# Kernel optimization log

Measured on AMD Instinct MI355X. Metric: run time of the kernel, lower is better.

## Reference

```python
import jax, jax.numpy as jnp
import numpy as np

N_NODES = 50000


def gcn_conv(x, row, col, ew, W, b, n_nodes):
    """PyG GCNConv: add self-loops, symmetric normalization, scatter-add aggregation."""
    loop = jnp.arange(n_nodes)
    r = jnp.concatenate([row, loop])
    c = jnp.concatenate([col, loop])
    w = jnp.concatenate([ew, jnp.ones((n_nodes,), ew.dtype)])
    deg = jax.ops.segment_sum(w, c, num_segments=n_nodes)          # [N]
    dinv = jnp.where(deg > 0, jax.lax.rsqrt(deg), 0.0)
    norm = dinv[r] * w * dinv[c]                                   # [E+N]
    h = x @ W                                                      # [N, out]
    msg = h[r] * norm[:, None]                                     # [E+N, out]
    out = jax.ops.segment_sum(msg, c, num_segments=n_nodes)        # [N, out]
    return out + b


def setup_inputs() -> dict:
    key = jax.random.key(0)
    ks = jax.random.split(key, 7)
    n_feats, hidden, n_classes, n_edges = 256, 128, 40, 800000
    x = jax.random.normal(ks[0], (N_NODES, n_feats), dtype=jnp.float32)
    edge_index = jax.random.randint(ks[1], (2, n_edges), 0, N_NODES, dtype=jnp.int64)
    edge_weight = jax.random.uniform(ks[2], (n_edges,), dtype=jnp.float32)
    # Glorot-ish init for the two GCNConv linear layers (weight stored as [in, out])
    W1 = jax.random.normal(ks[3], (n_feats, hidden), dtype=jnp.float32) * (1.0 / np.sqrt(n_feats))
    b1 = jnp.zeros((hidden,), dtype=jnp.float32)
    W2 = jax.random.normal(ks[4], (hidden, n_classes), dtype=jnp.float32) * (1.0 / np.sqrt(hidden))
    b2 = jnp.zeros((n_classes,), dtype=jnp.float32)
    return {"x": x, "edge_index": edge_index, "edge_weight": edge_weight,
            "W1": W1, "b1": b1, "W2": W2, "b2": b2}


def reference(x, edge_index, edge_weight, W1, b1, W2, b2):
    # Dropout is identity in eval mode.
    row, col = edge_index[0], edge_index[1]
    h = gcn_conv(x, row, col, edge_weight, W1, b1, N_NODES)
    h = jax.nn.relu(h)
    out = gcn_conv(h, row, col, edge_weight, W2, b2, N_NODES)
    return out
```

## Files before the change

kernel.cpp:

```cpp
#include <hip/hip_runtime.h>

#define N_FEATS 256
#define HIDDEN  128
#define NCLASS  40
#define H2PAD   48
#define ELLCAP  64

typedef __attribute__((ext_vector_type(8))) short short8;
typedef __attribute__((ext_vector_type(4))) float f32x4;

static __device__ __forceinline__ unsigned short f2bf(float f) {
    unsigned u = __float_as_uint(f);
    u += 0x7fffu + ((u >> 16) & 1u);
    return (unsigned short)(u >> 16);
}
static __device__ __forceinline__ float bflo(unsigned u) { return __uint_as_float(u << 16); }
static __device__ __forceinline__ float bfhi(unsigned u) { return __uint_as_float(u & 0xffff0000u); }

static __device__ __forceinline__ unsigned wq16(float w) {
    float q = w * 65536.0f + 0.5f;
    q = fminf(q, 65535.0f);
    return (unsigned)q;
}
#define WDEQ (1.0f / 65536.0f)

__global__ void k_convW(const float* __restrict__ W1, const float* __restrict__ W2,
                        unsigned short* __restrict__ Wp, unsigned short* __restrict__ Wp2,
                        unsigned long long* __restrict__ cntw, int N) {
    int idx = blockIdx.x * 256 + threadIdx.x;
    if (idx < N) cntw[idx] = 0ull;
    if (idx < N_FEATS * HIDDEN) {
        int n = idx >> 8, k = idx & 255;
        Wp[idx] = f2bf(W1[(size_t)k * HIDDEN + n]);
    } else {
        int j = idx - N_FEATS * HIDDEN;
        if (j < H2PAD * HIDDEN) {
            int n = j >> 7, k = j & 127;
            Wp2[j] = (n < NCLASS) ? f2bf(W2[(size_t)k * NCLASS + n]) : 0;
        }
    }
}

__global__ __launch_bounds__(256) void k_fat(const float* __restrict__ x,
                                             const unsigned short* __restrict__ Wp,
                                             unsigned short* __restrict__ C,
                                             const int* __restrict__ col,
                                             const int* __restrict__ row,
                                             const float* __restrict__ ew,
                                             unsigned long long* __restrict__ cntw,
                                             unsigned* __restrict__ ed,
                                             int GB, int CB, int N, int E) {
    int bid = blockIdx.x;
    int M = GB < CB ? GB : CB;
    int tile = -1, chunk = -1;
    if (bid < 2 * M) {
        if (bid & 1) chunk = bid >> 1; else tile = bid >> 1;
    } else {
        int r = bid - 2 * M;
        if (GB > CB) tile = M + r; else chunk = M + r;
    }

    if (tile >= 0) {
        __shared__ unsigned short Als[64][72];
        __shared__ unsigned short Bls[128][72];
        int t = threadIdx.x;
        int r0 = tile * 64;
        int wave = t >> 6, lane = t & 63;
        int ml = lane & 15, qd = lane >> 4;

        f32x4 acc[8];
        #pragma unroll
        for (int i = 0; i < 8; ++i) acc[i] = (f32x4){0.f, 0.f, 0.f, 0.f};

        int arow = t >> 2, akg = t & 3;
        int bn = t >> 1, bkg = t & 1;

        for (int k0 = 0; k0 < N_FEATS; k0 += 32) {
            {
                float4 xa0 = make_float4(0.f, 0.f, 0.f, 0.f), xa1 = xa0;
                if (r0 + arow < N) {
                    const float* src = &x[(size_t)(r0 + arow) * N_FEATS + k0 + akg * 8];
                    xa0 = *(const float4*)src;
                    xa1 = *(const float4*)(src + 4);
                }
                short8 av;
                av[0] = (short)f2bf(xa0.x); av[1] = (short)f2bf(xa0.y);
                av[2] = (short)f2bf(xa0.z); av[3] = (short)f2bf(xa0.w);
                av[4] = (short)f2bf(xa1.x); av[5] = (short)f2bf(xa1.y);
                av[6] = (short)f2bf(xa1.z); av[7] = (short)f2bf(xa1.w);
                *(short8*)&Als[arow][akg * 8] = av;
            }
            {
                const short8* src = (const short8*)&Wp[(size_t)bn * N_FEATS + k0 + bkg * 16];
                *(short8*)&Bls[bn][bkg * 16]     = src[0];
                *(short8*)&Bls[bn][bkg * 16 + 8] = src[1];
            }
            __syncthreads();
            short8 af = *(const short8*)&Als[wave * 16 + ml][qd * 8];
            #pragma unroll
            for (int nt = 0; nt < 8; ++nt) {
                short8 bf = *(const short8*)&Bls[nt * 16 + ml][qd * 8];
                acc[nt] = __builtin_amdgcn_mfma_f32_16x16x32_bf16(af, bf, acc[nt], 0, 0, 0);
            }
            __syncthreads();
        }
        #pragma unroll
        for (int nt = 0; nt < 8; ++nt) {
            int q = nt >> 1;
            int fo = (nt & 1) * 16 + ml;
            #pragma unroll
            for (int r = 0; r < 4; ++r) {
                int grow = r0 + wave * 16 + qd * 4 + r;
                if (grow < N)
                    C[(size_t)q * N * 32 + (size_t)grow * 32 + fo] = (unsigned short)f2bf(acc[nt][r]);
            }
        }
    } else {
        int base = chunk * 1024 + threadIdx.x * 4;
        if (base + 4 <= E) {
            int4   c4 = *(const int4*)&col[base];
            int4   r4 = *(const int4*)&row[base];
            float4 w4 = *(const float4*)&ew[base];
            unsigned q0 = wq16(w4.x), q1 = wq16(w4.y), q2 = wq16(w4.z), q3 = wq16(w4.w);
            unsigned p0 = ((unsigned)r4.x << 16) | q0;
            unsigned p1 = ((unsigned)r4.y << 16) | q1;
            unsigned p2 = ((unsigned)r4.z << 16) | q2;
            unsigned p3 = ((unsigned)r4.w << 16) | q3;
            unsigned long long a0 = atomicAdd(&cntw[c4.x], ((unsigned long long)q0 << 20) | 1ull);
            unsigned long long a1 = atomicAdd(&cntw[c4.y], ((unsigned long long)q1 << 20) | 1ull);
            unsigned long long a2 = atomicAdd(&cntw[c4.z], ((unsigned long long)q2 << 20) | 1ull);
            unsigned long long a3 = atomicAdd(&cntw[c4.w], ((unsigned long long)q3 << 20) | 1ull);
            int s0 = (int)(a0 & 0xFFFFFu);
            int s1 = (int)(a1 & 0xFFFFFu);
            int s2 = (int)(a2 & 0xFFFFFu);
            int s3 = (int)(a3 & 0xFFFFFu);
            if (s0 < ELLCAP) __builtin_nontemporal_store(p0, &ed[((size_t)c4.x << 6) + s0]);
            if (s1 < ELLCAP) __builtin_nontemporal_store(p1, &ed[((size_t)c4.y << 6) + s1]);
            if (s2 < ELLCAP) __builtin_nontemporal_store(p2, &ed[((size_t)c4.z << 6) + s2]);
            if (s3 < ELLCAP) __builtin_nontemporal_store(p3, &ed[((size_t)c4.w << 6) + s3]);
        } else {
            for (int e = base; e < E; ++e) {
                int c = col[e];
                unsigned q = wq16(ew[e]);
                unsigned p = ((unsigned)row[e] << 16) | q;
                unsigned long long a = atomicAdd(&cntw[c], ((unsigned long long)q << 20) | 1ull);
                int s = (int)(a & 0xFFFFFu);
                if (s < ELLCAP) __builtin_nontemporal_store(p, &ed[((size_t)c << 6) + s]);
            }
        }
    }
}

__global__ void k_degdinv(const unsigned long long* __restrict__ cntw,
                          float* __restrict__ dinv, int* __restrict__ cnt, int N) {
    int c = blockIdx.x * blockDim.x + threadIdx.x;
    if (c >= N) return;
    unsigned long long v = cntw[c];
    int m = (int)(v & 0xFFFFFu); if (m > ELLCAP) m = ELLCAP;
    cnt[c] = m;
    dinv[c] = rsqrtf(1.0f + (float)(v >> 20) * WDEQ);
}

__global__ __launch_bounds__(256) void k_gather1(const int* __restrict__ cnt,
                                                 const unsigned* __restrict__ ed,
                                                 const unsigned short* __restrict__ h,
                                                 const float* __restrict__ dinv,
                                                 const float* __restrict__ b1,
                                                 const unsigned short* __restrict__ Wp2,
                                                 unsigned short* __restrict__ h2b, int N) {
    __shared__ unsigned short Ah[16][136];
    int t = threadIdx.x;
    int wave = t >> 6, lane = t & 63;
    int nl = lane >> 4;
    int sub = lane & 15;
    int g = sub >> 2;
    int f2 = sub & 3;
    int c0 = blockIdx.x * 16;
    int node = wave * 4 + nl;
    int c = c0 + node;
    const uint4* hb = (const uint4*)h;

    bool valid = c < N;
    int m = valid ? cnt[c] : 0;
    const unsigned* ep = ed + ((size_t)c << 6);
    float dc = valid ? dinv[c] : 0.f;
    float sl = dc * dc;

    #pragma unroll
    for (int q = 0; q < 4; ++q) {
        const uint4* hq = hb + (size_t)q * N * 4;
        float acc[8] = {};
        int i = 0;
        for (; i + 8 <= m; i += 8) {
            unsigned e0 = ep[i + g], e1 = ep[i + 4 + g];
            uint4 v0 = hq[(size_t)(e0 >> 16) * 4 + f2];
            uint4 v1 = hq[(size_t)(e1 >> 16) * 4 + f2];
            float w0 = (float)(e0 & 0xffffu) * WDEQ * dinv[e0 >> 16];
            float w1 = (float)(e1 & 0xffffu) * WDEQ * dinv[e1 >> 16];
            acc[0] += w0 * bflo(v0.x); acc[1] += w0 * bfhi(v0.x);
            acc[2] += w0 * bflo(v0.y); acc[3] += w0 * bfhi(v0.y);
            acc[4] += w0 * bflo(v0.z); acc[5] += w0 * bfhi(v0.z);
            acc[6] += w0 * bflo(v0.w); acc[7] += w0 * bfhi(v0.w);
            acc[0] += w1 * bflo(v1.x); acc[1] += w1 * bfhi(v1.x);
            acc[2] += w1 * bflo(v1.y); acc[3] += w1 * bfhi(v1.y);
            acc[4] += w1 * bflo(v1.z); acc[5] += w1 * bfhi(v1.z);
            acc[6] += w1 * bflo(v1.w); acc[7] += w1 * bfhi(v1.w);
        }
        if (i + g < m) {
            unsigned e0 = ep[i + g];
            uint4 v0 = hq[(size_t)(e0 >> 16) * 4 + f2];
            float w0 = (float)(e0 & 0xffffu) * WDEQ * dinv[e0 >> 16];
            acc[0] += w0 * bflo(v0.x); acc[1] += w0 * bfhi(v0.x);
            acc[2] += w0 * bflo(v0.y); acc[3] += w0 * bfhi(v0.y);
            acc[4] += w0 * bflo(v0.z); acc[5] += w0 * bfhi(v0.z);
            acc[6] += w0 * bflo(v0.w); acc[7] += w0 * bfhi(v0.w);
        }
        if (i + 4 + g < m) {
            unsigned e1 = ep[i + 4 + g];
            uint4 v1 = hq[(size_t)(e1 >> 16) * 4 + f2];
            float w1 = (float)(e1 & 0xffffu) * WDEQ * dinv[e1 >> 16];
            acc[0] += w1 * bflo(v1.x); acc[1] += w1 * bfhi(v1.x);
            acc[2] += w1 * bflo(v1.y); acc[3] += w1 * bfhi(v1.y);
            acc[4] += w1 * bflo(v1.z); acc[5] += w1 * bfhi(v1.z);
            acc[6] += w1 * bflo(v1.w); acc[7] += w1 * bfhi(v1.w);
        }
        #pragma unroll
        for (int j = 0; j < 8; ++j) acc[j] += __shfl_xor(acc[j], 4, 64);
        #pragma unroll
        for (int j = 0; j < 8; ++j) acc[j] += __shfl_xor(acc[j], 8, 64);

        short8 ov = {};
        if (valid) {
            uint4 hv = hq[(size_t)c * 4 + f2];
            float4 ba = *(const float4*)&b1[q * 32 + f2 * 8];
            float4 bb = *(const float4*)&b1[q * 32 + f2 * 8 + 4];
            float o[8];
            o[0] = dc * acc[0] + sl * bflo(hv.x) + ba.x;
            o[1] = dc * acc[1] + sl * bfhi(hv.x) + ba.y;
            o[2] = dc * acc[2] + sl * bflo(hv.y) + ba.z;
            o[3] = dc * acc[3] + sl * bfhi(hv.y) + ba.w;
            o[4] = dc * acc[4] + sl * bflo(hv.z) + bb.x;
            o[5] = dc * acc[5] + sl * bfhi(hv.z) + bb.y;
            o[6] = dc * acc[6] + sl * bflo(hv.w) + bb.z;
            o[7] = dc * acc[7] + sl * bfhi(hv.w) + bb.w;
            #pragma unroll
            for (int j = 0; j < 8; ++j) {
                float v = o[j] > 0.f ? o[j] : 0.f;
                ov[j] = (short)f2bf(v);
            }
        }
        if (g == 0) *(short8*)&Ah[node][q * 32 + f2 * 8] = ov;
    }
    __syncthreads();

    if (t < 64) {
        int ml = t & 15, qd = t >> 4;
        f32x4 acc2[3];
        #pragma unroll
        for (int i = 0; i < 3; ++i) acc2[i] = (f32x4){0.f, 0.f, 0.f, 0.f};
        #pragma unroll
        for (int ks = 0; ks < 4; ++ks) {
            short8 af = *(const short8*)&Ah[ml][ks * 32 + qd * 8];
            #pragma unroll
            for (int nt = 0; nt < 3; ++nt) {
                short8 bf = *(const short8*)&Wp2[(size_t)(nt * 16 + ml) * HIDDEN + ks * 32 + qd * 8];
                acc2[nt] = __builtin_amdgcn_mfma_f32_16x16x32_bf16(af, bf, acc2[nt], 0, 0, 0);
            }
        }
        #pragma unroll
        for (int nt = 0; nt < 3; ++nt) {
            int j = nt * 16 + ml;
            #pragma unroll
            for (int r = 0; r < 4; ++r) {
                int gr = c0 + qd * 4 + r;
                if (gr < N) h2b[(size_t)gr * H2PAD + j] = (unsigned short)f2bf(acc2[nt][r]);
            }
        }
    }
}

__global__ __launch_bounds__(256) void k_gather2(const int* __restrict__ cnt,
                                                 const unsigned* __restrict__ ed,
                                                 const unsigned short* __restrict__ h,
                                                 const float* __restrict__ dinv,
                                                 const float* __restrict__ b2,
                                                 float* __restrict__ out, int N) {
    int t = threadIdx.x;
    int wave = t >> 6, lane = t & 63;
    int g = lane >> 3, s = lane & 7;
    int c = blockIdx.x * 4 + wave;
    if (c >= N) return;
    const uint4* hb = (const uint4*)h;
    bool act = s < 6;
    int m = cnt[c];
    const unsigned* ep = ed + ((size_t)c << 6);
    float acc[8] = {};
    int i = 0;
    for (; i + 16 <= m; i += 16) {
        unsigned e0 = ep[i + g], e1 = ep[i + g + 8];
        float w0 = (float)(e0 & 0xffffu) * WDEQ * dinv[e0 >> 16];
        float w1 = (float)(e1 & 0xffffu) * WDEQ * dinv[e1 >> 16];
        if (act) {
            uint4 v0 = hb[(size_t)(e0 >> 16) * 6 + s];
            uint4 v1 = hb[(size_t)(e1 >> 16) * 6 + s];
            acc[0] += w0 * bflo(v0.x); acc[1] += w0 * bfhi(v0.x);
            acc[2] += w0 * bflo(v0.y); acc[3] += w0 * bfhi(v0.y);
            acc[4] += w0 * bflo(v0.z); acc[5] += w0 * bfhi(v0.z);
            acc[6] += w0 * bflo(v0.w); acc[7] += w0 * bfhi(v0.w);
            acc[0] += w1 * bflo(v1.x); acc[1] += w1 * bfhi(v1.x);
            acc[2] += w1 * bflo(v1.y); acc[3] += w1 * bfhi(v1.y);
            acc[4] += w1 * bflo(v1.z); acc[5] += w1 * bfhi(v1.z);
            acc[6] += w1 * bflo(v1.w); acc[7] += w1 * bfhi(v1.w);
        }
    }
    if (i + g < m) {
        unsigned e0 = ep[i + g];
        float w0 = (float)(e0 & 0xffffu) * WDEQ * dinv[e0 >> 16];
        if (act) {
            uint4 v0 = hb[(size_t)(e0 >> 16) * 6 + s];
            acc[0] += w0 * bflo(v0.x); acc[1] += w0 * bfhi(v0.x);
            acc[2] += w0 * bflo(v0.y); acc[3] += w0 * bfhi(v0.y);
            acc[4] += w0 * bflo(v0.z); acc[5] += w0 * bfhi(v0.z);
            acc[6] += w0 * bflo(v0.w); acc[7] += w0 * bfhi(v0.w);
        }
    }
    if (i + g + 8 < m) {
        unsigned e1 = ep[i + g + 8];
        float w1 = (float)(e1 & 0xffffu) * WDEQ * dinv[e1 >> 16];
        if (act) {
            uint4 v1 = hb[(size_t)(e1 >> 16) * 6 + s];
            acc[0] += w1 * bflo(v1.x); acc[1] += w1 * bfhi(v1.x);
            acc[2] += w1 * bflo(v1.y); acc[3] += w1 * bfhi(v1.y);
            acc[4] += w1 * bflo(v1.z); acc[5] += w1 * bfhi(v1.z);
            acc[6] += w1 * bflo(v1.w); acc[7] += w1 * bfhi(v1.w);
        }
    }
    #pragma unroll
    for (int j = 0; j < 8; ++j) acc[j] += __shfl_xor(acc[j], 8, 64);
    #pragma unroll
    for (int j = 0; j < 8; ++j) acc[j] += __shfl_xor(acc[j], 16, 64);
    #pragma unroll
    for (int j = 0; j < 8; ++j) acc[j] += __shfl_xor(acc[j], 32, 64);

    if (g == 0 && s < 5) {
        float dc = dinv[c], sl = dc * dc;
        uint4 hv = hb[(size_t)c * 6 + s];
        float4 ba = *(const float4*)&b2[s * 8];
        float4 bb = *(const float4*)&b2[s * 8 + 4];
        float4 oa, ob;
        oa.x = dc * acc[0] + sl * bflo(hv.x) + ba.x;
        oa.y = dc * acc[1] + sl * bfhi(hv.x) + ba.y;
        oa.z = dc * acc[2] + sl * bflo(hv.y) + ba.z;
        oa.w = dc * acc[3] + sl * bfhi(hv.y) + ba.w;
        ob.x = dc * acc[4] + sl * bflo(hv.z) + bb.x;
        ob.y = dc * acc[5] + sl * bfhi(hv.z) + bb.y;
        ob.z = dc * acc[6] + sl * bflo(hv.w) + bb.z;
        ob.w = dc * acc[7] + sl * bfhi(hv.w) + bb.w;
        *(float4*)&out[(size_t)c * NCLASS + s * 8]     = oa;
        *(float4*)&out[(size_t)c * NCLASS + s * 8 + 4] = ob;
    }
}

extern "C" void kernel_launch(void* const* d_in, const int* in_sizes, int n_in,
                              void* d_out, int out_size, void* d_ws, size_t ws_size,
                              hipStream_t stream) {
    const float* x  = (const float*)d_in[0];
    const int*   ei = (const int*)d_in[1];
    const float* ew = (const float*)d_in[2];
    const float* W1 = (const float*)d_in[3];
    const float* b1 = (const float*)d_in[4];
    const float* W2 = (const float*)d_in[5];
    const float* b2 = (const float*)d_in[6];
    float* out = (float*)d_out;

    const int E = in_sizes[2];
    const int N = in_sizes[0] / N_FEATS;
    const int* row = ei;
    const int* col = ei + E;

    unsigned long long* cntw = (unsigned long long*)d_ws;
    float* dinv = (float*)(cntw + N);
    int*   cnt  = (int*)(dinv + N);
    unsigned* ed = (unsigned*)(cnt + N);
    unsigned short* Wp  = (unsigned short*)(ed + (size_t)N * ELLCAP);
    unsigned short* Wp2 = Wp + (size_t)N_FEATS * HIDDEN;
    unsigned short* h1b = Wp2 + H2PAD * HIDDEN;
    unsigned short* h2b = h1b + (size_t)N * HIDDEN;

    {
        int nw = N_FEATS * HIDDEN + H2PAD * HIDDEN;
        int total = N > nw ? N : nw;
        k_convW<<<(total + 255) / 256, 256, 0, stream>>>(W1, W2, Wp, Wp2, cntw, N);
    }

    {
        int GB = (N + 63) / 64;
        int CB = (E + 1023) / 1024;
        k_fat<<<GB + CB, 256, 0, stream>>>(x, Wp, h1b, col, row, ew, cntw, ed, GB, CB, N, E);
    }

    k_degdinv<<<(N + 255) / 256, 256, 0, stream>>>(cntw, dinv, cnt, N);

    k_gather1<<<(N + 15) / 16, 256, 0, stream>>>(cnt, ed, h1b, dinv, b1, Wp2, h2b, N);

    k_gather2<<<(N + 3) / 4, 256, 0, stream>>>(cnt, ed, h2b, dinv, b2, out, N);
}
```

Measured before the change: 213.4 us.

## Drop degree kernel; recompute dinv from packed counters and retune cache hints

Removes the separate k_degdinv launch. The gather kernels now read the packed 64-bit count/weight word and compute rsqrt and the clamped count inline, including for every neighbour. It also makes the x loads and the h1 stores non-temporal, and turns the ELL edge stores back into normal cached stores. This saves a launch and the dinv/cnt arrays, but each neighbour now needs an 8-byte gather and an extra rsqrt instead of a 4-byte one.

```diff
diff --git a/kernel.cpp b/kernel.cpp
--- a/kernel.cpp
+++ b/kernel.cpp
@@ -23,6 +23,14 @@
     return (unsigned)q;
 }
 #define WDEQ (1.0f / 65536.0f)
+
+static __device__ __forceinline__ float dinv_of(unsigned long long v) {
+    return rsqrtf(1.0f + (float)(v >> 20) * WDEQ);
+}
+static __device__ __forceinline__ int m_of(unsigned long long v) {
+    int m = (int)(v & 0xFFFFFu);
+    return m > ELLCAP ? ELLCAP : m;
+}
 
 __global__ void k_convW(const float* __restrict__ W1, const float* __restrict__ W2,
                         unsigned short* __restrict__ Wp, unsigned short* __restrict__ Wp2,
@@ -77,11 +85,11 @@
 
         for (int k0 = 0; k0 < N_FEATS; k0 += 32) {
             {
-                float4 xa0 = make_float4(0.f, 0.f, 0.f, 0.f), xa1 = xa0;
+                f32x4 xa0 = (f32x4){0.f, 0.f, 0.f, 0.f}, xa1 = xa0;
                 if (r0 + arow < N) {
-                    const float* src = &x[(size_t)(r0 + arow) * N_FEATS + k0 + akg * 8];
-                    xa0 = *(const float4*)src;
-                    xa1 = *(const float4*)(src + 4);
+                    const f32x4* src = (const f32x4*)&x[(size_t)(r0 + arow) * N_FEATS + k0 + akg * 8];
+                    xa0 = __builtin_nontemporal_load(src);
+                    xa1 = __builtin_nontemporal_load(src + 1);
                 }
                 short8 av;
                 av[0] = (short)f2bf(xa0.x); av[1] = (short)f2bf(xa0.y);
@@ -112,7 +120,8 @@
             for (int r = 0; r < 4; ++r) {
                 int grow = r0 + wave * 16 + qd * 4 + r;
                 if (grow < N)
-                    C[(size_t)q * N * 32 + (size_t)grow * 32 + fo] = (unsigned short)f2bf(acc[nt][r]);
+                    __builtin_nontemporal_store((unsigned short)f2bf(acc[nt][r]),
+                        &C[(size_t)q * N * 32 + (size_t)grow * 32 + fo]);
             }
         }
     } else {
@@ -134,10 +143,10 @@
             int s1 = (int)(a1 & 0xFFFFFu);
             int s2 = (int)(a2 & 0xFFFFFu);
             int s3 = (int)(a3 & 0xFFFFFu);
-            if (s0 < ELLCAP) __builtin_nontemporal_store(p0, &ed[((size_t)c4.x << 6) + s0]);
-            if (s1 < ELLCAP) __builtin_nontemporal_store(p1, &ed[((size_t)c4.y << 6) + s1]);
-            if (s2 < ELLCAP) __builtin_nontemporal_store(p2, &ed[((size_t)c4.z << 6) + s2]);
-            if (s3 < ELLCAP) __builtin_nontemporal_store(p3, &ed[((size_t)c4.w << 6) + s3]);
+            if (s0 < ELLCAP) ed[((size_t)c4.x << 6) + s0] = p0;
+            if (s1 < ELLCAP) ed[((size_t)c4.y << 6) + s1] = p1;
+            if (s2 < ELLCAP) ed[((size_t)c4.z << 6) + s2] = p2;
+            if (s3 < ELLCAP) ed[((size_t)c4.w << 6) + s3] = p3;
         } else {
             for (int e = base; e < E; ++e) {
                 int c = col[e];
@@ -145,26 +154,15 @@
                 unsigned p = ((unsigned)row[e] << 16) | q;
                 unsigned long long a = atomicAdd(&cntw[c], ((unsigned long long)q << 20) | 1ull);
                 int s = (int)(a & 0xFFFFFu);
-                if (s < ELLCAP) __builtin_nontemporal_store(p, &ed[((size_t)c << 6) + s]);
-            }
-        }
-    }
-}
-
-__global__ void k_degdinv(const unsigned long long* __restrict__ cntw,
-                          float* __restrict__ dinv, int* __restrict__ cnt, int N) {
-    int c = blockIdx.x * blockDim.x + threadIdx.x;
-    if (c >= N) return;
-    unsigned long long v = cntw[c];
-    int m = (int)(v & 0xFFFFFu); if (m > ELLCAP) m = ELLCAP;
-    cnt[c] = m;
-    dinv[c] = rsqrtf(1.0f + (float)(v >> 20) * WDEQ);
-}
-
-__global__ __launch_bounds__(256) void k_gather1(const int* __restrict__ cnt,
+                if (s < ELLCAP) ed[((size_t)c << 6) + s] = p;
+            }
+        }
+    }
+}
+
+__global__ __launch_bounds__(256) void k_gather1(const unsigned long long* __restrict__ cntw,
                                                  const unsigned* __restrict__ ed,
                                                  const unsigned short* __restrict__ h,
-                                                 const float* __restrict__ dinv,
                                                  const float* __restrict__ b1,
                                                  const unsigned short* __restrict__ Wp2,
                                                  unsigned short* __restrict__ h2b, int N) {
@@ -181,9 +179,10 @@
     const uint4* hb = (const uint4*)h;
 
     bool valid = c < N;
-    int m = valid ? cnt[c] : 0;
+    unsigned long long vc = valid ? cntw[c] : 0ull;
+    int m = valid ? m_of(vc) : 0;
     const unsigned* ep = ed + ((size_t)c << 6);
-    float dc = valid ? dinv[c] : 0.f;
+    float dc = valid ? dinv_of(vc) : 0.f;
     float sl = dc * dc;
 
     #pragma unroll
@@ -195,8 +194,8 @@
             unsigned e0 = ep[i + g], e1 = ep[i + 4 + g];
             uint4 v0 = hq[(size_t)(e0 >> 16) * 4 + f2];
             uint4 v1 = hq[(size_t)(e1 >> 16) * 4 + f2];
-            float w0 = (float)(e0 & 0xffffu) * WDEQ * dinv[e0 >> 16];
-            float w1 = (float)(e1 & 0xffffu) * WDEQ * dinv[e1 >> 16];
+            float w0 = (float)(e0 & 0xffffu) * WDEQ * dinv_of(cntw[e0 >> 16]);
+            float w1 = (float)(e1 & 0xffffu) * WDEQ * dinv_of(cntw[e1 >> 16]);
             acc[0] += w0 * bflo(v0.x); acc[1] += w0 * bfhi(v0.x);
             acc[2] += w0 * bflo(v0.y); acc[3] += w0 * bfhi(v0.y);
             acc[4] += w0 * bflo(v0.z); acc[5] += w0 * bfhi(v0.z);
@@ -209,7 +208,7 @@
         if (i + g < m) {
             unsigned e0 = ep[i + g];
             uint4 v0 = hq[(size_t)(e0 >> 16) * 4 + f2];
-            float w0 = (float)(e0 & 0xffffu) * WDEQ * dinv[e0 >> 16];
+            float w0 = (float)(e0 & 0xffffu) * WDEQ * dinv_of(cntw[e0 >> 16]);
             acc[0] += w0 * bflo(v0.x); acc[1] += w0 * bfhi(v0.x);
             acc[2] += w0 * bflo(v0.y); acc[3] += w0 * bfhi(v0.y);
             acc[4] += w0 * bflo(v0.z); acc[5] += w0 * bfhi(v0.z);
@@ -218,7 +217,7 @@
         if (i + 4 + g < m) {
             unsigned e1 = ep[i + 4 + g];
             uint4 v1 = hq[(size_t)(e1 >> 16) * 4 + f2];
-            float w1 = (float)(e1 & 0xffffu) * WDEQ * dinv[e1 >> 16];
+            float w1 = (float)(e1 & 0xffffu) * WDEQ * dinv_of(cntw[e1 >> 16]);
             acc[0] += w1 * bflo(v1.x); acc[1] += w1 * bfhi(v1.x);
             acc[2] += w1 * bflo(v1.y); acc[3] += w1 * bfhi(v1.y);
             acc[4] += w1 * bflo(v1.z); acc[5] += w1 * bfhi(v1.z);
@@ -279,10 +278,9 @@
     }
 }
 
-__global__ __launch_bounds__(256) void k_gather2(const int* __restrict__ cnt,
+__global__ __launch_bounds__(256) void k_gather2(const unsigned long long* __restrict__ cntw,
                                                  const unsigned* __restrict__ ed,
                                                  const unsigned short* __restrict__ h,
-                                                 const float* __restrict__ dinv,
                                                  const float* __restrict__ b2,
                                                  float* __restrict__ out, int N) {
     int t = threadIdx.x;
@@ -292,14 +290,16 @@
     if (c >= N) return;
     const uint4* hb = (const uint4*)h;
     bool act = s < 6;
-    int m = cnt[c];
+    unsigned long long vc = cntw[c];
+    int m = m_of(vc);
+    float dc = dinv_of(vc);
     const unsigned* ep = ed + ((size_t)c << 6);
     float acc[8] = {};
     int i = 0;
     for (; i + 16 <= m; i += 16) {
         unsigned e0 = ep[i + g], e1 = ep[i + g + 8];
-        float w0 = (float)(e0 & 0xffffu) * WDEQ * dinv[e0 >> 16];
-        float w1 = (float)(e1 & 0xffffu) * WDEQ * dinv[e1 >> 16];
+        float w0 = (float)(e0 & 0xffffu) * WDEQ * dinv_of(cntw[e0 >> 16]);
+        float w1 = (float)(e1 & 0xffffu) * WDEQ * dinv_of(cntw[e1 >> 16]);
         if (act) {
             uint4 v0 = hb[(size_t)(e0 >> 16) * 6 + s];
             uint4 v1 = hb[(size_t)(e1 >> 16) * 6 + s];
@@ -315,7 +315,7 @@
     }
     if (i + g < m) {
         unsigned e0 = ep[i + g];
-        float w0 = (float)(e0 & 0xffffu) * WDEQ * dinv[e0 >> 16];
+        float w0 = (float)(e0 & 0xffffu) * WDEQ * dinv_of(cntw[e0 >> 16]);
         if (act) {
             uint4 v0 = hb[(size_t)(e0 >> 16) * 6 + s];
             acc[0] += w0 * bflo(v0.x); acc[1] += w0 * bfhi(v0.x);
@@ -326,7 +326,7 @@
     }
     if (i + g + 8 < m) {
         unsigned e1 = ep[i + g + 8];
-        float w1 = (float)(e1 & 0xffffu) * WDEQ * dinv[e1 >> 16];
+        float w1 = (float)(e1 & 0xffffu) * WDEQ * dinv_of(cntw[e1 >> 16]);
         if (act) {
             uint4 v1 = hb[(size_t)(e1 >> 16) * 6 + s];
             acc[0] += w1 * bflo(v1.x); acc[1] += w1 * bfhi(v1.x);
@@ -343,7 +343,7 @@
     for (int j = 0; j < 8; ++j) acc[j] += __shfl_xor(acc[j], 32, 64);
 
     if (g == 0 && s < 5) {
-        float dc = dinv[c], sl = dc * dc;
+        float sl = dc * dc;
         uint4 hv = hb[(size_t)c * 6 + s];
         float4 ba = *(const float4*)&b2[s * 8];
         float4 bb = *(const float4*)&b2[s * 8 + 4];
@@ -379,9 +379,7 @@
     const int* col = ei + E;
 
     unsigned long long* cntw = (unsigned long long*)d_ws;
-    float* dinv = (float*)(cntw + N);
-    int*   cnt  = (int*)(dinv + N);
-    unsigned* ed = (unsigned*)(cnt + N);
+    unsigned* ed = (unsigned*)(cntw + N);
     unsigned short* Wp  = (unsigned short*)(ed + (size_t)N * ELLCAP);
     unsigned short* Wp2 = Wp + (size_t)N_FEATS * HIDDEN;
     unsigned short* h1b = Wp2 + H2PAD * HIDDEN;
@@ -399,9 +397,7 @@
         k_fat<<<GB + CB, 256, 0, stream>>>(x, Wp, h1b, col, row, ew, cntw, ed, GB, CB, N, E);
     }
 
-    k_degdinv<<<(N + 255) / 256, 256, 0, stream>>>(cntw, dinv, cnt, N);
-
-    k_gather1<<<(N + 15) / 16, 256, 0, stream>>>(cnt, ed, h1b, dinv, b1, Wp2, h2b, N);
-
-    k_gather2<<<(N + 3) / 4, 256, 0, stream>>>(cnt, ed, h2b, dinv, b2, out, N);
-}
+    k_gather1<<<(N + 15) / 16, 256, 0, stream>>>(cntw, ed, h1b, b1, Wp2, h2b, N);
+
+    k_gather2<<<(N + 3) / 4, 256, 0, stream>>>(cntw, ed, h2b, b2, out, N);
+}
```

Result: slower. 238.9 us (+12.0%).

## Split layer-1 gather by feature quarter with XCD-aware block mapping, separate GEMM2

Applied to the files above, without the earlier changes.

The layer-1 gather now handles one 32-feature quarter per block, and each quarter is pinned to a pair of XCDs through the block-index mapping. This keeps each XCD's L2 working set to one quarter of the h1 table, reducing random-gather misses. The fused MFMA projection is split out into a new k_gemm2 kernel that reads an intermediate bf16 aggregate buffer. The cost is an extra kernel launch, an extra N×128 bf16 write and read, and edge lists and dinv that are now read four times.

```diff
diff --git a/kernel.cpp b/kernel.cpp
--- a/kernel.cpp
+++ b/kernel.cpp
@@ -161,120 +161,127 @@
     dinv[c] = rsqrtf(1.0f + (float)(v >> 20) * WDEQ);
 }
 
-__global__ __launch_bounds__(256) void k_gather1(const int* __restrict__ cnt,
-                                                 const unsigned* __restrict__ ed,
-                                                 const unsigned short* __restrict__ h,
-                                                 const float* __restrict__ dinv,
-                                                 const float* __restrict__ b1,
-                                                 const unsigned short* __restrict__ Wp2,
-                                                 unsigned short* __restrict__ h2b, int N) {
-    __shared__ unsigned short Ah[16][136];
+__global__ __launch_bounds__(256) void k_gather1q(const int* __restrict__ cnt,
+                                                  const unsigned* __restrict__ ed,
+                                                  const unsigned short* __restrict__ h,
+                                                  const float* __restrict__ dinv,
+                                                  const float* __restrict__ b1,
+                                                  unsigned short* __restrict__ agg,
+                                                  int N, int NG) {
+    int bid = blockIdx.x;
+    int xcd = bid & 7;
+    int q = xcd >> 1;
+    int ng = (bid >> 3) * 2 + (xcd & 1);
+    if (ng >= NG) return;
     int t = threadIdx.x;
-    int wave = t >> 6, lane = t & 63;
-    int nl = lane >> 4;
-    int sub = lane & 15;
+    int nl = t >> 3;
+    int sub = t & 7;
     int g = sub >> 2;
     int f2 = sub & 3;
-    int c0 = blockIdx.x * 16;
-    int node = wave * 4 + nl;
-    int c = c0 + node;
-    const uint4* hb = (const uint4*)h;
-
+    int c = ng * 32 + nl;
     bool valid = c < N;
+    const uint4* hq = (const uint4*)h + (size_t)q * N * 4;
+
     int m = valid ? cnt[c] : 0;
     const unsigned* ep = ed + ((size_t)c << 6);
-    float dc = valid ? dinv[c] : 0.f;
-    float sl = dc * dc;
-
-    #pragma unroll
-    for (int q = 0; q < 4; ++q) {
-        const uint4* hq = hb + (size_t)q * N * 4;
-        float acc[8] = {};
-        int i = 0;
-        for (; i + 8 <= m; i += 8) {
-            unsigned e0 = ep[i + g], e1 = ep[i + 4 + g];
-            uint4 v0 = hq[(size_t)(e0 >> 16) * 4 + f2];
-            uint4 v1 = hq[(size_t)(e1 >> 16) * 4 + f2];
-            float w0 = (float)(e0 & 0xffffu) * WDEQ * dinv[e0 >> 16];
-            float w1 = (float)(e1 & 0xffffu) * WDEQ * dinv[e1 >> 16];
-            acc[0] += w0 * bflo(v0.x); acc[1] += w0 * bfhi(v0.x);
-            acc[2] += w0 * bflo(v0.y); acc[3] += w0 * bfhi(v0.y);
-            acc[4] += w0 * bflo(v0.z); acc[5] += w0 * bfhi(v0.z);
-            acc[6] += w0 * bflo(v0.w); acc[7] += w0 * bfhi(v0.w);
-            acc[0] += w1 * bflo(v1.x); acc[1] += w1 * bfhi(v1.x);
-            acc[2] += w1 * bflo(v1.y); acc[3] += w1 * bfhi(v1.y);
-            acc[4] += w1 * bflo(v1.z); acc[5] += w1 * bfhi(v1.z);
-            acc[6] += w1 * bflo(v1.w); acc[7] += w1 * bfhi(v1.w);
-        }
-        if (i + g < m) {
-            unsigned e0 = ep[i + g];
-            uint4 v0 = hq[(size_t)(e0 >> 16) * 4 + f2];
-            float w0 = (float)(e0 & 0xffffu) * WDEQ * dinv[e0 >> 16];
-            acc[0] += w0 * bflo(v0.x); acc[1] += w0 * bfhi(v0.x);
-            acc[2] += w0 * bflo(v0.y); acc[3] += w0 * bfhi(v0.y);
-            acc[4] += w0 * bflo(v0.z); acc[5] += w0 * bfhi(v0.z);
-            acc[6] += w0 * bflo(v0.w); acc[7] += w0 * bfhi(v0.w);
-        }
-        if (i + 4 + g < m) {
-            unsigned e1 = ep[i + 4 + g];
-            uint4 v1 = hq[(size_t)(e1 >> 16) * 4 + f2];
-            float w1 = (float)(e1 & 0xffffu) * WDEQ * dinv[e1 >> 16];
-            acc[0] += w1 * bflo(v1.x); acc[1] += w1 * bfhi(v1.x);
-            acc[2] += w1 * bflo(v1.y); acc[3] += w1 * bfhi(v1.y);
-            acc[4] += w1 * bflo(v1.z); acc[5] += w1 * bfhi(v1.z);
-            acc[6] += w1 * bflo(v1.w); acc[7] += w1 * bfhi(v1.w);
-        }
+    float acc[8] = {};
+    int i = 0;
+    for (; i + 4 <= m; i += 4) {
+        unsigned e0 = ep[i + g], e1 = ep[i + 2 + g];
+        uint4 v0 = hq[(size_t)(e0 >> 16) * 4 + f2];
+        uint4 v1 = hq[(size_t)(e1 >> 16) * 4 + f2];
+        float w0 = (float)(e0 & 0xffffu) * WDEQ * dinv[e0 >> 16];
+        float w1 = (float)(e1 & 0xffffu) * WDEQ * dinv[e1 >> 16];
+        acc[0] += w0 * bflo(v0.x); acc[1] += w0 * bfhi(v0.x);
+        acc[2] += w0 * bflo(v0.y); acc[3] += w0 * bfhi(v0.y);
+        acc[4] += w0 * bflo(v0.z); acc[5] += w0 * bfhi(v0.z);
+        acc[6] += w0 * bflo(v0.w); acc[7] += w0 * bfhi(v0.w);
+        acc[0] += w1 * bflo(v1.x); acc[1] += w1 * bfhi(v1.x);
+        acc[2] += w1 * bflo(v1.y); acc[3] += w1 * bfhi(v1.y);
+        acc[4] += w1 * bflo(v1.z); acc[5] += w1 * bfhi(v1.z);
+        acc[6] += w1 * bflo(v1.w); acc[7] += w1 * bfhi(v1.w);
+    }
+    if (i + g < m) {
+        unsigned e0 = ep[i + g];
+        uint4 v0 = hq[(size_t)(e0 >> 16) * 4 + f2];
+        float w0 = (float)(e0 & 0xffffu) * WDEQ * dinv[e0 >> 16];
+        acc[0] += w0 * bflo(v0.x); acc[1] += w0 * bfhi(v0.x);
+        acc[2] += w0 * bflo(v0.y); acc[3] += w0 * bfhi(v0.y);
+        acc[4] += w0 * bflo(v0.z); acc[5] += w0 * bfhi(v0.z);
+        acc[6] += w0 * bflo(v0.w); acc[7] += w0 * bfhi(v0.w);
+    }
+    if (i + 2 + g < m) {
+        unsigned e1 = ep[i + 2 + g];
+        uint4 v1 = hq[(size_t)(e1 >> 16) * 4 + f2];
+        float w1 = (float)(e1 & 0xffffu) * WDEQ * dinv[e1 >> 16];
+        acc[0] += w1 * bflo(v1.x); acc[1] += w1 * bfhi(v1.x);
+        acc[2] += w1 * bflo(v1.y); acc[3] += w1 * bfhi(v1.y);
+        acc[4] += w1 * bflo(v1.z); acc[5] += w1 * bfhi(v1.z);
+        acc[6] += w1 * bflo(v1.w); acc[7] += w1 * bfhi(v1.w);
+    }
+    #pragma unroll
+    for (int j = 0; j < 8; ++j) acc[j] += __shfl_xor(acc[j], 4, 64);
+
+    if (valid && g == 0) {
+        float dc = dinv[c], sl = dc * dc;
+        uint4 hv = hq[(size_t)c * 4 + f2];
+        float4 ba = *(const float4*)&b1[q * 32 + f2 * 8];
+        float4 bb = *(const float4*)&b1[q * 32 + f2 * 8 + 4];
+        float o[8];
+        o[0] = dc * acc[0] + sl * bflo(hv.x) + ba.x;
+        o[1] = dc * acc[1] + sl * bfhi(hv.x) + ba.y;
+        o[2] = dc * acc[2] + sl * bflo(hv.y) + ba.z;
+        o[3] = dc * acc[3] + sl * bfhi(hv.y) + ba.w;
+        o[4] = dc * acc[4] + sl * bflo(hv.z) + bb.x;
+        o[5] = dc * acc[5] + sl * bfhi(hv.z) + bb.y;
+        o[6] = dc * acc[6] + sl * bflo(hv.w) + bb.z;
+        o[7] = dc * acc[7] + sl * bfhi(hv.w) + bb.w;
+        short8 ov;
         #pragma unroll
-        for (int j = 0; j < 8; ++j) acc[j] += __shfl_xor(acc[j], 4, 64);
-        #pragma unroll
-        for (int j = 0; j < 8; ++j) acc[j] += __shfl_xor(acc[j], 8, 64);
-
-        short8 ov = {};
-        if (valid) {
-            uint4 hv = hq[(size_t)c * 4 + f2];
-            float4 ba = *(const float4*)&b1[q * 32 + f2 * 8];
-            float4 bb = *(const float4*)&b1[q * 32 + f2 * 8 + 4];
-            float o[8];
-            o[0] = dc * acc[0] + sl * bflo(hv.x) + ba.x;
-            o[1] = dc * acc[1] + sl * bfhi(hv.x) + ba.y;
-            o[2] = dc * acc[2] + sl * bflo(hv.y) + ba.z;
-            o[3] = dc * acc[3] + sl * bfhi(hv.y) + ba.w;
-            o[4] = dc * acc[4] + sl * bflo(hv.z) + bb.x;
-            o[5] = dc * acc[5] + sl * bfhi(hv.z) + bb.y;
-            o[6] = dc * acc[6] + sl * bflo(hv.w) + bb.z;
-            o[7] = dc * acc[7] + sl * bfhi(hv.w) + bb.w;
-            #pragma unroll
-            for (int j = 0; j < 8; ++j) {
-                float v = o[j] > 0.f ? o[j] : 0.f;
-                ov[j] = (short)f2bf(v);
-            }
-        }
-        if (g == 0) *(short8*)&Ah[node][q * 32 + f2 * 8] = ov;
+        for (int j = 0; j < 8; ++j) {
+            float v = o[j] > 0.f ? o[j] : 0.f;
+            ov[j] = (short)f2bf(v);
+        }
+        *(short8*)&agg[(size_t)c * HIDDEN + q * 32 + f2 * 8] = ov;
+    }
+}
+
+__global__ __launch_bounds__(256) void k_gemm2(const unsigned short* __restrict__ agg,
+                                               const unsigned short* __restrict__ Wp2,
+                                               unsigned short* __restrict__ h2b, int N) {
+    __shared__ unsigned short Als[64][136];
+    int t = threadIdx.x;
+    int r0 = blockIdx.x * 64;
+    int arow = t >> 2, akg = t & 3;
+    if (r0 + arow < N) {
+        const short8* src = (const short8*)&agg[(size_t)(r0 + arow) * HIDDEN + akg * 32];
+        *(short8*)&Als[arow][akg * 32]      = src[0];
+        *(short8*)&Als[arow][akg * 32 + 8]  = src[1];
+        *(short8*)&Als[arow][akg * 32 + 16] = src[2];
+        *(short8*)&Als[arow][akg * 32 + 24] = src[3];
     }
     __syncthreads();
-
-    if (t < 64) {
-        int ml = t & 15, qd = t >> 4;
-        f32x4 acc2[3];
-        #pragma unroll
-        for (int i = 0; i < 3; ++i) acc2[i] = (f32x4){0.f, 0.f, 0.f, 0.f};
-        #pragma unroll
-        for (int ks = 0; ks < 4; ++ks) {
-            short8 af = *(const short8*)&Ah[ml][ks * 32 + qd * 8];
-            #pragma unroll
-            for (int nt = 0; nt < 3; ++nt) {
-                short8 bf = *(const short8*)&Wp2[(size_t)(nt * 16 + ml) * HIDDEN + ks * 32 + qd * 8];
-                acc2[nt] = __builtin_amdgcn_mfma_f32_16x16x32_bf16(af, bf, acc2[nt], 0, 0, 0);
-            }
-        }
+    int wave = t >> 6, lane = t & 63;
+    int ml = lane & 15, qd = lane >> 4;
+    f32x4 acc2[3];
+    #pragma unroll
+    for (int i = 0; i < 3; ++i) acc2[i] = (f32x4){0.f, 0.f, 0.f, 0.f};
+    #pragma unroll
+    for (int ks = 0; ks < 4; ++ks) {
+        short8 af = *(const short8*)&Als[wave * 16 + ml][ks * 32 + qd * 8];
         #pragma unroll
         for (int nt = 0; nt < 3; ++nt) {
-            int j = nt * 16 + ml;
-            #pragma unroll
-            for (int r = 0; r < 4; ++r) {
-                int gr = c0 + qd * 4 + r;
-                if (gr < N) h2b[(size_t)gr * H2PAD + j] = (unsigned short)f2bf(acc2[nt][r]);
-            }
+            short8 bf = *(const short8*)&Wp2[(size_t)(nt * 16 + ml) * HIDDEN + ks * 32 + qd * 8];
+            acc2[nt] = __builtin_amdgcn_mfma_f32_16x16x32_bf16(af, bf, acc2[nt], 0, 0, 0);
+        }
+    }
+    #pragma unroll
+    for (int nt = 0; nt < 3; ++nt) {
+        int j = nt * 16 + ml;
+        #pragma unroll
+        for (int r = 0; r < 4; ++r) {
+            int gr = r0 + wave * 16 + qd * 4 + r;
+            if (gr < N) h2b[(size_t)gr * H2PAD + j] = (unsigned short)f2bf(acc2[nt][r]);
         }
     }
 }
@@ -384,8 +391,9 @@
     unsigned* ed = (unsigned*)(cnt + N);
     unsigned short* Wp  = (unsigned short*)(ed + (size_t)N * ELLCAP);
     unsigned short* Wp2 = Wp + (size_t)N_FEATS * HIDDEN;
-    unsigned short* h1b = Wp2 + H2PAD * HIDDEN;
-    unsigned short* h2b = h1b + (size_t)N * HIDDEN;
+    unsigned short* h1q = Wp2 + H2PAD * HIDDEN;
+    unsigned short* agg = h1q + (size_t)N * HIDDEN;
+    unsigned short* h2b = agg + (size_t)N * HIDDEN;
 
     {
         int nw = N_FEATS * HIDDEN + H2PAD * HIDDEN;
@@ -396,12 +404,18 @@
     {
         int GB = (N + 63) / 64;
         int CB = (E + 1023) / 1024;
-        k_fat<<<GB + CB, 256, 0, stream>>>(x, Wp, h1b, col, row, ew, cntw, ed, GB, CB, N, E);
+        k_fat<<<GB + CB, 256, 0, stream>>>(x, Wp, h1q, col, row, ew, cntw, ed, GB, CB, N, E);
     }
 
     k_degdinv<<<(N + 255) / 256, 256, 0, stream>>>(cntw, dinv, cnt, N);
 
-    k_gather1<<<(N + 15) / 16, 256, 0, stream>>>(cnt, ed, h1b, dinv, b1, Wp2, h2b, N);
+    {
+        int NG = (N + 31) / 32;
+        int G = ((4 * NG + 7) / 8) * 8;
+        k_gather1q<<<G, 256, 0, stream>>>(cnt, ed, h1q, dinv, b1, agg, N, NG);
+    }
+
+    k_gemm2<<<(N + 63) / 64, 256, 0, stream>>>(agg, Wp2, h2b, N);
 
     k_gather2<<<(N + 3) / 4, 256, 0, stream>>>(cnt, ed, h2b, dinv, b2, out, N);
 }
```

Measured after the change: 217.2 us. About the same (+1.8%).
